# Optimization experiments

Hardware: AMD Instinct MI355X
Metric: run time of the kernel (lower is better)

The kernel has to match this reference:

```python
import jax, jax.numpy as jnp
import numpy as np

L_NOOBJ = 3.0


def _scale_loss(pred, gt, modulus, mask_pos, mask_neg):
    # pred/gt: [B,H,W,A,5+C]; modulus: [B,H,W,A,6]; mask_pos: [B,H,W,A] bool; mask_neg: same shape as pred, bool
    C = pred.shape[-1] - 5
    mpos = mask_pos.astype(pred.dtype)[..., None]           # broadcast over channel dim
    n_pos = jnp.sum(mask_pos)
    n_pos_f = jnp.maximum(n_pos, 1).astype(pred.dtype)
    # modulus weight of the LAST positive cell (reproduces box_param[ground_index][0] after the loop)
    flat = mask_pos.reshape(-1)
    idx_last = flat.shape[0] - 1 - jnp.argmax(flat[::-1])
    w_last = modulus.reshape(-1, 6)[idx_last, 0]
    diff2 = (gt - pred) ** 2 * mpos
    coord = w_last * jnp.sum(diff2[..., 0:4]) / n_pos_f
    conf_pos = jnp.sum(diff2[..., 4]) / n_pos_f
    # BCEWithLogitsLoss (mean over selected rows x C elements), numerically stable form
    x = pred[..., 5:]
    z = gt[..., 5:]
    bce = jnp.maximum(x, 0.0) - x * z + jnp.log1p(jnp.exp(-jnp.abs(x)))
    classify = jnp.sum(bce * mpos) / (n_pos_f * C)
    pos_loss = jnp.where(n_pos > 0, coord + conf_pos + classify, 0.0)
    # negative: elementwise masked MSE over full tensor, scaled by l_noobj
    mneg = mask_neg.astype(pred.dtype)
    n_neg = jnp.sum(mask_neg)
    neg = L_NOOBJ * jnp.sum(((gt - pred) ** 2) * mneg) / jnp.maximum(n_neg, 1).astype(pred.dtype)
    neg_loss = jnp.where(n_neg > 0, neg, 0.0)
    return pos_loss + neg_loss


def setup_inputs() -> dict:
    key = jax.random.key(0)
    B, A, C = 16, 3, 80
    sizes = {"small": 76, "middle": 38, "big": 19}
    out = {}
    k = key
    for name, g in sizes.items():
        k, k1, k2, k3, k4, k5 = jax.random.split(k, 6)
        out[f"{name}_pred"] = jax.random.normal(k1, (B, g, g, A, 5 + C), dtype=jnp.float32)
        out[f"{name}_gt"] = jax.random.uniform(k2, (B, g, g, A, 5 + C), dtype=jnp.float32)
        out[f"{name}_modulus"] = jax.random.uniform(k3, (B, g, g, A, 6), dtype=jnp.float32) + 0.5
        out[f"{name}_mask_pos"] = jax.random.bernoulli(k4, 0.01, (B, g, g, A))
        out[f"{name}_mask_neg"] = jax.random.bernoulli(k5, 0.3, (B, g, g, A, 5 + C))
    return out


def reference(small_pred, small_gt, small_modulus, small_mask_pos, small_mask_neg,
              middle_pred, middle_gt, middle_modulus, middle_mask_pos, middle_mask_neg,
              big_pred, big_gt, big_modulus, big_mask_pos, big_mask_neg):
    loss = (_scale_loss(small_pred, small_gt, small_modulus, small_mask_pos, small_mask_neg)
            + _scale_loss(middle_pred, middle_gt, middle_modulus, middle_mask_pos, middle_mask_neg)
            + _scale_loss(big_pred, big_gt, big_modulus, big_mask_pos, big_mask_neg))
    return loss
```

## Files before the change

kernel.cpp:

```cpp
#include <hip/hip_runtime.h>

typedef unsigned int u32;
typedef unsigned long long u64;

#define NG0 5891520u
#define NG1 1472880u
#define NG2 368220u
#define NC0 277248u
#define NC1 69312u
#define NC2 17328u
#define NBLK 2048u
#define PB0 1083u
#define PB1 271u
#define PB2 68u
#define PBTOT (PB0 + PB1 + PB2)

struct NegAcc { float sn; u32 nn; };
struct PosAcc { float sc, sf, sb; u32 np, mi, pad[3]; };


__device__ __forceinline__ void neg_body(const float4 pv, const float4 gv,
                                         const int4 mv, float& sn, u32& nn)
{
  float d;
  d = gv.x - pv.x; sn = fmaf(d * d, (float)mv.x, sn); nn += (u32)mv.x;
  d = gv.y - pv.y; sn = fmaf(d * d, (float)mv.y, sn); nn += (u32)mv.y;
  d = gv.z - pv.z; sn = fmaf(d * d, (float)mv.z, sn); nn += (u32)mv.z;
  d = gv.w - pv.w; sn = fmaf(d * d, (float)mv.w, sn); nn += (u32)mv.w;
}

__device__ __forceinline__ void neg_scale(
    const float* __restrict__ pred, const float* __restrict__ gt,
    const int* __restrict__ mneg, u32 n, u32 tid, u32 stride,
    NegAcc* __restrict__ slot)
{
  const float4* __restrict__ p4 = (const float4*)pred;
  const float4* __restrict__ g4 = (const float4*)gt;
  const int4*   __restrict__ m4 = (const int4*)mneg;
  float sn = 0.f; u32 nn = 0;
  const u32 iters = n / stride;
  u32 i = 0;
  for (; i + 4 <= iters; i += 4) {
    u32 g0 = tid + i * stride, g1 = g0 + stride, g2 = g1 + stride, g3 = g2 + stride;
    float4 pa = p4[g0], pb = p4[g1], pc = p4[g2], pd = p4[g3];
    float4 qa = g4[g0], qb = g4[g1], qc = g4[g2], qd = g4[g3];
    int4   ma = m4[g0], mb = m4[g1], mc = m4[g2], md = m4[g3];
    neg_body(pa, qa, ma, sn, nn);
    neg_body(pb, qb, mb, sn, nn);
    neg_body(pc, qc, mc, sn, nn);
    neg_body(pd, qd, md, sn, nn);
  }
  for (; i < iters; ++i) {
    u32 ga = tid + i * stride;
    neg_body(p4[ga], g4[ga], m4[ga], sn, nn);
  }
  u32 gl = tid + iters * stride;
  if (gl < n) {
    neg_body(p4[gl], g4[gl], m4[gl], sn, nn);
  }
  #pragma unroll
  for (int o = 32; o > 0; o >>= 1) {
    sn += __shfl_down(sn, o);
    nn += __shfl_down((int)nn, o);
  }
  __shared__ float shf[4];
  __shared__ u32 shu[4];
  const int wave = threadIdx.x >> 6, lane = threadIdx.x & 63;
  if (lane == 0) { shf[wave] = sn; shu[wave] = nn; }
  __syncthreads();
  if (threadIdx.x == 0) {
    NegAcc a;
    a.sn = shf[0] + shf[1] + shf[2] + shf[3];
    a.nn = shu[0] + shu[1] + shu[2] + shu[3];
    *slot = a;
  }
  __syncthreads();
}

__global__ __launch_bounds__(256) void yolo_neg(
    const float* __restrict__ pred0, const float* __restrict__ gt0, const int* __restrict__ mn0,
    const float* __restrict__ pred1, const float* __restrict__ gt1, const int* __restrict__ mn1,
    const float* __restrict__ pred2, const float* __restrict__ gt2, const int* __restrict__ mn2,
    NegAcc* __restrict__ neg)
{
  const u32 tid = blockIdx.x * blockDim.x + threadIdx.x;
  const u32 stride = gridDim.x * blockDim.x;
  neg_scale(pred0, gt0, mn0, NG0, tid, stride, &neg[0 * NBLK + blockIdx.x]);
  neg_scale(pred1, gt1, mn1, NG1, tid, stride, &neg[1 * NBLK + blockIdx.x]);
  neg_scale(pred2, gt2, mn2, NG2, tid, stride, &neg[2 * NBLK + blockIdx.x]);
}


__global__ __launch_bounds__(256) void yolo_pos(
    const float* __restrict__ pred0, const float* __restrict__ gt0, const int* __restrict__ mp0,
    const float* __restrict__ pred1, const float* __restrict__ gt1, const int* __restrict__ mp1,
    const float* __restrict__ pred2, const float* __restrict__ gt2, const int* __restrict__ mp2,
    PosAcc* __restrict__ pos)
{
  const u32 b = blockIdx.x;
  const float* pred; const float* gtp; const int* mp; u32 nc, cell0;
  if (b < PB0)            { pred = pred0; gtp = gt0; mp = mp0; nc = NC0; cell0 = b * 256u; }
  else if (b < PB0 + PB1) { pred = pred1; gtp = gt1; mp = mp1; nc = NC1; cell0 = (b - PB0) * 256u; }
  else                    { pred = pred2; gtp = gt2; mp = mp2; nc = NC2; cell0 = (b - PB0 - PB1) * 256u; }

  const int lane = threadIdx.x & 63;
  const int wave = threadIdx.x >> 6;
  const u32 cell = cell0 + threadIdx.x;
  const u32 wavecell0 = cell0 + (u32)(threadIdx.x & ~63u);

  const bool active = (cell < nc) && (mp[cell] != 0);
  u64 bal = __ballot(active);

  float sc = 0.f, sf = 0.f, sb = 0.f;
  u32 np = active ? 1u : 0u;
  u32 mi = active ? cell : 0u;

  while (bal) {
    const int src = __ffsll(bal) - 1;
    bal &= bal - 1ull;
    const u32 c = wavecell0 + (u32)src;
    const float* __restrict__ pp = pred + (size_t)c * 85u;
    const float* __restrict__ gg = gtp  + (size_t)c * 85u;
    float x0 = pp[lane], z0 = gg[lane];
    float d0 = z0 - x0;
    float b0 = fmaxf(x0, 0.f) - x0 * z0 + __logf(1.f + __expf(-fabsf(x0)));
    if (lane < 4)       sc += d0 * d0;
    else if (lane == 4) sf += d0 * d0;
    else                sb += b0;
    if (lane < 21) {
      float x1 = pp[64 + lane], z1 = gg[64 + lane];
      sb += fmaxf(x1, 0.f) - x1 * z1 + __logf(1.f + __expf(-fabsf(x1)));
    }
  }

  #pragma unroll
  for (int o = 32; o > 0; o >>= 1) {
    sc += __shfl_down(sc, o);
    sf += __shfl_down(sf, o);
    sb += __shfl_down(sb, o);
    np += __shfl_down((int)np, o);
    u32 om = __shfl_down((int)mi, o);
    mi = om > mi ? om : mi;
  }
  __shared__ float shf[3][4];
  __shared__ u32 shu[2][4];
  if (lane == 0) {
    shf[0][wave] = sc; shf[1][wave] = sf; shf[2][wave] = sb;
    shu[0][wave] = np; shu[1][wave] = mi;
  }
  __syncthreads();
  if (threadIdx.x == 0) {
    PosAcc a = {0.f, 0.f, 0.f, 0u, 0u, {0u, 0u, 0u}};
    #pragma unroll
    for (int w = 0; w < 4; ++w) {
      a.sc += shf[0][w]; a.sf += shf[1][w]; a.sb += shf[2][w];
      a.np += shu[0][w];
      a.mi = shu[1][w] > a.mi ? shu[1][w] : a.mi;
    }
    pos[b] = a;
  }
}


__global__ __launch_bounds__(256) void yolo_final(
    const NegAcc* __restrict__ neg, const PosAcc* __restrict__ pos,
    const float* __restrict__ mod0, const float* __restrict__ mod1,
    const float* __restrict__ mod2, float* __restrict__ out)
{
  const float* mods[3] = {mod0, mod1, mod2};
  const u32 pbase[3] = {0u, PB0, PB0 + PB1};
  const u32 pcnt[3]  = {PB0, PB1, PB2};
  __shared__ float shf[4][4];
  __shared__ u32 shu[3][4];
  const int wave = threadIdx.x >> 6, lane = threadIdx.x & 63;
  float loss = 0.f;
  for (int s = 0; s < 3; ++s) {
    float sn = 0.f, sc = 0.f, sf = 0.f, sb = 0.f;
    u32 nn = 0, np = 0, mi = 0;
    for (u32 t = threadIdx.x; t < NBLK; t += 256u) {
      NegAcc a = neg[(u32)s * NBLK + t];
      sn += a.sn; nn += a.nn;
    }
    for (u32 t = threadIdx.x; t < pcnt[s]; t += 256u) {
      PosAcc a = pos[pbase[s] + t];
      sc += a.sc; sf += a.sf; sb += a.sb; np += a.np;
      mi = a.mi > mi ? a.mi : mi;
    }
    #pragma unroll
    for (int o = 32; o > 0; o >>= 1) {
      sn += __shfl_down(sn, o);
      sc += __shfl_down(sc, o);
      sf += __shfl_down(sf, o);
      sb += __shfl_down(sb, o);
      nn += __shfl_down((int)nn, o);
      np += __shfl_down((int)np, o);
      u32 om = __shfl_down((int)mi, o);
      mi = om > mi ? om : mi;
    }
    if (lane == 0) {
      shf[0][wave] = sn; shf[1][wave] = sc; shf[2][wave] = sf; shf[3][wave] = sb;
      shu[0][wave] = nn; shu[1][wave] = np; shu[2][wave] = mi;
    }
    __syncthreads();
    if (threadIdx.x == 0) {
      float Sn = 0.f, Sc = 0.f, Sf = 0.f, Sb = 0.f;
      u32 Nn = 0, Np = 0, Mi = 0;
      #pragma unroll
      for (int w = 0; w < 4; ++w) {
        Sn += shf[0][w]; Sc += shf[1][w]; Sf += shf[2][w]; Sb += shf[3][w];
        Nn += shu[0][w]; Np += shu[1][w];
        Mi = shu[2][w] > Mi ? shu[2][w] : Mi;
      }
      if (Np > 0u) {
        float w_last = mods[s][(size_t)Mi * 6u];
        loss += (w_last * Sc + Sf + Sb * (1.f / 80.f)) / (float)Np;
      }
      if (Nn > 0u) loss += 3.0f * Sn / (float)Nn;
    }
    __syncthreads();
  }
  if (threadIdx.x == 0) out[0] = loss;
}

extern "C" void kernel_launch(void* const* d_in, const int* in_sizes, int n_in,
                              void* d_out, int out_size, void* d_ws, size_t ws_size,
                              hipStream_t stream)
{
  const float* pred0 = (const float*)d_in[0];
  const float* gt0   = (const float*)d_in[1];
  const float* mod0  = (const float*)d_in[2];
  const int*   mp0   = (const int*)d_in[3];
  const int*   mn0   = (const int*)d_in[4];
  const float* pred1 = (const float*)d_in[5];
  const float* gt1   = (const float*)d_in[6];
  const float* mod1  = (const float*)d_in[7];
  const int*   mp1   = (const int*)d_in[8];
  const int*   mn1   = (const int*)d_in[9];
  const float* pred2 = (const float*)d_in[10];
  const float* gt2   = (const float*)d_in[11];
  const float* mod2  = (const float*)d_in[12];
  const int*   mp2   = (const int*)d_in[13];
  const int*   mn2   = (const int*)d_in[14];

  NegAcc* neg = (NegAcc*)d_ws;
  PosAcc* pos = (PosAcc*)((char*)d_ws + 3 * NBLK * sizeof(NegAcc));

  yolo_neg<<<NBLK, 256, 0, stream>>>(pred0, gt0, mn0,
                                     pred1, gt1, mn1,
                                     pred2, gt2, mn2, neg);
  yolo_pos<<<PBTOT, 256, 0, stream>>>(pred0, gt0, mp0,
                                      pred1, gt1, mp1,
                                      pred2, gt2, mp2, pos);
  yolo_final<<<1, 256, 0, stream>>>(neg, pos, mod0, mod1, mod2, (float*)d_out);
}
```

Before: 88.64 us.

## Fuse negative and positive loss kernels into one launch with single-wave finalize

After: 86.43 us. 1.03x faster.

```diff
diff --git a/kernel.cpp b/kernel.cpp
--- a/kernel.cpp
+++ b/kernel.cpp
@@ -15,9 +15,13 @@
 #define PB2 68u
 #define PBTOT (PB0 + PB1 + PB2)
 
-struct NegAcc { float sn; u32 nn; };
-struct PosAcc { float sc, sf, sb; u32 np, mi, pad[3]; };
-
+struct BlockAcc {
+  float sn0, sn1, sn2;
+  u32   nn0, nn1, nn2;
+  float sc, sf, sb;
+  u32   np, mi;
+  u32   pad[5];
+};
 
 __device__ __forceinline__ void neg_body(const float4 pv, const float4 gv,
                                          const int4 mv, float& sn, u32& nn)
@@ -29,197 +33,185 @@
   d = gv.w - pv.w; sn = fmaf(d * d, (float)mv.w, sn); nn += (u32)mv.w;
 }
 
-__device__ __forceinline__ void neg_scale(
+__device__ __forceinline__ void neg_stream(
     const float* __restrict__ pred, const float* __restrict__ gt,
     const int* __restrict__ mneg, u32 n, u32 tid, u32 stride,
-    NegAcc* __restrict__ slot)
+    float& sn, u32& nn)
 {
   const float4* __restrict__ p4 = (const float4*)pred;
   const float4* __restrict__ g4 = (const float4*)gt;
   const int4*   __restrict__ m4 = (const int4*)mneg;
-  float sn = 0.f; u32 nn = 0;
   const u32 iters = n / stride;
   u32 i = 0;
-  for (; i + 4 <= iters; i += 4) {
-    u32 g0 = tid + i * stride, g1 = g0 + stride, g2 = g1 + stride, g3 = g2 + stride;
-    float4 pa = p4[g0], pb = p4[g1], pc = p4[g2], pd = p4[g3];
-    float4 qa = g4[g0], qb = g4[g1], qc = g4[g2], qd = g4[g3];
-    int4   ma = m4[g0], mb = m4[g1], mc = m4[g2], md = m4[g3];
+  for (; i + 2 <= iters; i += 2) {
+    u32 ga = tid + i * stride, gb = ga + stride;
+    float4 pa = p4[ga], qa = g4[ga]; int4 ma = m4[ga];
+    float4 pb = p4[gb], qb = g4[gb]; int4 mb = m4[gb];
     neg_body(pa, qa, ma, sn, nn);
     neg_body(pb, qb, mb, sn, nn);
-    neg_body(pc, qc, mc, sn, nn);
-    neg_body(pd, qd, md, sn, nn);
-  }
-  for (; i < iters; ++i) {
+  }
+  if (i < iters) {
     u32 ga = tid + i * stride;
     neg_body(p4[ga], g4[ga], m4[ga], sn, nn);
   }
   u32 gl = tid + iters * stride;
-  if (gl < n) {
-    neg_body(p4[gl], g4[gl], m4[gl], sn, nn);
-  }
+  if (gl < n) neg_body(p4[gl], g4[gl], m4[gl], sn, nn);
+}
+
+__global__ __launch_bounds__(256) void yolo_fused(
+    const float* __restrict__ pred0, const float* __restrict__ gt0,
+    const int* __restrict__ mp0, const int* __restrict__ mn0,
+    const float* __restrict__ pred1, const float* __restrict__ gt1,
+    const int* __restrict__ mp1, const int* __restrict__ mn1,
+    const float* __restrict__ pred2, const float* __restrict__ gt2,
+    const int* __restrict__ mp2, const int* __restrict__ mn2,
+    BlockAcc* __restrict__ ws)
+{
+  const u32 tid = blockIdx.x * blockDim.x + threadIdx.x;
+  const u32 stride = gridDim.x * blockDim.x;
+
+  float sn0 = 0.f, sn1 = 0.f, sn2 = 0.f;
+  u32 nn0 = 0, nn1 = 0, nn2 = 0;
+  neg_stream(pred0, gt0, mn0, NG0, tid, stride, sn0, nn0);
+  neg_stream(pred1, gt1, mn1, NG1, tid, stride, sn1, nn1);
+  neg_stream(pred2, gt2, mn2, NG2, tid, stride, sn2, nn2);
+
+  float sc = 0.f, sf = 0.f, sb = 0.f;
+  u32 np = 0, mi = 0;
+  const u32 b = blockIdx.x;
+  if (b < PBTOT) {
+    const float* pred; const float* gtp; const int* mp; u32 nc, cell0;
+    if (b < PB0)            { pred = pred0; gtp = gt0; mp = mp0; nc = NC0; cell0 = b * 256u; }
+    else if (b < PB0 + PB1) { pred = pred1; gtp = gt1; mp = mp1; nc = NC1; cell0 = (b - PB0) * 256u; }
+    else                    { pred = pred2; gtp = gt2; mp = mp2; nc = NC2; cell0 = (b - PB0 - PB1) * 256u; }
+
+    const int lane = threadIdx.x & 63;
+    const u32 cell = cell0 + threadIdx.x;
+    const u32 wavecell0 = cell0 + (u32)(threadIdx.x & ~63u);
+    const bool active = (cell < nc) && (mp[cell] != 0);
+    u64 bal = __ballot(active);
+    np = active ? 1u : 0u;
+    mi = active ? cell : 0u;
+
+    while (bal) {
+      const int src = __ffsll(bal) - 1;
+      bal &= bal - 1ull;
+      const u32 c = wavecell0 + (u32)src;
+      const float* __restrict__ pp = pred + (size_t)c * 85u;
+      const float* __restrict__ gg = gtp  + (size_t)c * 85u;
+      float x0 = pp[lane], z0 = gg[lane];
+      float d0 = z0 - x0;
+      float b0 = fmaxf(x0, 0.f) - x0 * z0 + __logf(1.f + __expf(-fabsf(x0)));
+      if (lane < 4)       sc += d0 * d0;
+      else if (lane == 4) sf += d0 * d0;
+      else                sb += b0;
+      if (lane < 21) {
+        float x1 = pp[64 + lane], z1 = gg[64 + lane];
+        sb += fmaxf(x1, 0.f) - x1 * z1 + __logf(1.f + __expf(-fabsf(x1)));
+      }
+    }
+  }
+
   #pragma unroll
   for (int o = 32; o > 0; o >>= 1) {
-    sn += __shfl_down(sn, o);
-    nn += __shfl_down((int)nn, o);
-  }
-  __shared__ float shf[4];
-  __shared__ u32 shu[4];
+    sn0 += __shfl_down(sn0, o);
+    sn1 += __shfl_down(sn1, o);
+    sn2 += __shfl_down(sn2, o);
+    nn0 += __shfl_down((int)nn0, o);
+    nn1 += __shfl_down((int)nn1, o);
+    nn2 += __shfl_down((int)nn2, o);
+    sc  += __shfl_down(sc, o);
+    sf  += __shfl_down(sf, o);
+    sb  += __shfl_down(sb, o);
+    np  += __shfl_down((int)np, o);
+    u32 om = __shfl_down((int)mi, o);
+    mi = om > mi ? om : mi;
+  }
+  __shared__ float shf[6][4];
+  __shared__ u32 shu[5][4];
   const int wave = threadIdx.x >> 6, lane = threadIdx.x & 63;
-  if (lane == 0) { shf[wave] = sn; shu[wave] = nn; }
+  if (lane == 0) {
+    shf[0][wave] = sn0; shf[1][wave] = sn1; shf[2][wave] = sn2;
+    shf[3][wave] = sc;  shf[4][wave] = sf;  shf[5][wave] = sb;
+    shu[0][wave] = nn0; shu[1][wave] = nn1; shu[2][wave] = nn2;
+    shu[3][wave] = np;  shu[4][wave] = mi;
+  }
   __syncthreads();
   if (threadIdx.x == 0) {
-    NegAcc a;
-    a.sn = shf[0] + shf[1] + shf[2] + shf[3];
-    a.nn = shu[0] + shu[1] + shu[2] + shu[3];
-    *slot = a;
-  }
-  __syncthreads();
-}
-
-__global__ __launch_bounds__(256) void yolo_neg(
-    const float* __restrict__ pred0, const float* __restrict__ gt0, const int* __restrict__ mn0,
-    const float* __restrict__ pred1, const float* __restrict__ gt1, const int* __restrict__ mn1,
-    const float* __restrict__ pred2, const float* __restrict__ gt2, const int* __restrict__ mn2,
-    NegAcc* __restrict__ neg)
-{
-  const u32 tid = blockIdx.x * blockDim.x + threadIdx.x;
-  const u32 stride = gridDim.x * blockDim.x;
-  neg_scale(pred0, gt0, mn0, NG0, tid, stride, &neg[0 * NBLK + blockIdx.x]);
-  neg_scale(pred1, gt1, mn1, NG1, tid, stride, &neg[1 * NBLK + blockIdx.x]);
-  neg_scale(pred2, gt2, mn2, NG2, tid, stride, &neg[2 * NBLK + blockIdx.x]);
-}
-
-
-__global__ __launch_bounds__(256) void yolo_pos(
-    const float* __restrict__ pred0, const float* __restrict__ gt0, const int* __restrict__ mp0,
-    const float* __restrict__ pred1, const float* __restrict__ gt1, const int* __restrict__ mp1,
-    const float* __restrict__ pred2, const float* __restrict__ gt2, const int* __restrict__ mp2,
-    PosAcc* __restrict__ pos)
-{
-  const u32 b = blockIdx.x;
-  const float* pred; const float* gtp; const int* mp; u32 nc, cell0;
-  if (b < PB0)            { pred = pred0; gtp = gt0; mp = mp0; nc = NC0; cell0 = b * 256u; }
-  else if (b < PB0 + PB1) { pred = pred1; gtp = gt1; mp = mp1; nc = NC1; cell0 = (b - PB0) * 256u; }
-  else                    { pred = pred2; gtp = gt2; mp = mp2; nc = NC2; cell0 = (b - PB0 - PB1) * 256u; }
-
-  const int lane = threadIdx.x & 63;
-  const int wave = threadIdx.x >> 6;
-  const u32 cell = cell0 + threadIdx.x;
-  const u32 wavecell0 = cell0 + (u32)(threadIdx.x & ~63u);
-
-  const bool active = (cell < nc) && (mp[cell] != 0);
-  u64 bal = __ballot(active);
-
-  float sc = 0.f, sf = 0.f, sb = 0.f;
-  u32 np = active ? 1u : 0u;
-  u32 mi = active ? cell : 0u;
-
-  while (bal) {
-    const int src = __ffsll(bal) - 1;
-    bal &= bal - 1ull;
-    const u32 c = wavecell0 + (u32)src;
-    const float* __restrict__ pp = pred + (size_t)c * 85u;
-    const float* __restrict__ gg = gtp  + (size_t)c * 85u;
-    float x0 = pp[lane], z0 = gg[lane];
-    float d0 = z0 - x0;
-    float b0 = fmaxf(x0, 0.f) - x0 * z0 + __logf(1.f + __expf(-fabsf(x0)));
-    if (lane < 4)       sc += d0 * d0;
-    else if (lane == 4) sf += d0 * d0;
-    else                sb += b0;
-    if (lane < 21) {
-      float x1 = pp[64 + lane], z1 = gg[64 + lane];
-      sb += fmaxf(x1, 0.f) - x1 * z1 + __logf(1.f + __expf(-fabsf(x1)));
+    BlockAcc a = {};
+    #pragma unroll
+    for (int w = 0; w < 4; ++w) {
+      a.sn0 += shf[0][w]; a.sn1 += shf[1][w]; a.sn2 += shf[2][w];
+      a.sc  += shf[3][w]; a.sf  += shf[4][w]; a.sb  += shf[5][w];
+      a.nn0 += shu[0][w]; a.nn1 += shu[1][w]; a.nn2 += shu[2][w];
+      a.np  += shu[3][w];
+      a.mi = shu[4][w] > a.mi ? shu[4][w] : a.mi;
     }
+    ws[blockIdx.x] = a;
+  }
+}
+
+__global__ __launch_bounds__(64) void yolo_final(
+    const BlockAcc* __restrict__ ws,
+    const float* __restrict__ mod0, const float* __restrict__ mod1,
+    const float* __restrict__ mod2, float* __restrict__ out)
+{
+  const int lane = threadIdx.x;
+  float sn0 = 0.f, sn1 = 0.f, sn2 = 0.f;
+  float nn0 = 0.f, nn1 = 0.f, nn2 = 0.f;
+  u32 in0 = 0, in1 = 0, in2 = 0;
+  for (u32 t = lane; t < NBLK; t += 64u) {
+    const BlockAcc a = ws[t];
+    sn0 += a.sn0; sn1 += a.sn1; sn2 += a.sn2;
+    in0 += a.nn0; in1 += a.nn1; in2 += a.nn2;
+  }
+  nn0 = (float)in0; nn1 = (float)in1; nn2 = (float)in2;
+
+  float sc0 = 0.f, sf0 = 0.f, sb0 = 0.f; u32 np0 = 0, mi0 = 0;
+  for (u32 t = lane; t < PB0; t += 64u) {
+    const BlockAcc a = ws[t];
+    sc0 += a.sc; sf0 += a.sf; sb0 += a.sb; np0 += a.np;
+    mi0 = a.mi > mi0 ? a.mi : mi0;
+  }
+  float sc1 = 0.f, sf1 = 0.f, sb1 = 0.f; u32 np1 = 0, mi1 = 0;
+  for (u32 t = PB0 + lane; t < PB0 + PB1; t += 64u) {
+    const BlockAcc a = ws[t];
+    sc1 += a.sc; sf1 += a.sf; sb1 += a.sb; np1 += a.np;
+    mi1 = a.mi > mi1 ? a.mi : mi1;
+  }
+  float sc2 = 0.f, sf2 = 0.f, sb2 = 0.f; u32 np2 = 0, mi2 = 0;
+  for (u32 t = PB0 + PB1 + lane; t < PBTOT; t += 64u) {
+    const BlockAcc a = ws[t];
+    sc2 += a.sc; sf2 += a.sf; sb2 += a.sb; np2 += a.np;
+    mi2 = a.mi > mi2 ? a.mi : mi2;
   }
 
   #pragma unroll
   for (int o = 32; o > 0; o >>= 1) {
-    sc += __shfl_down(sc, o);
-    sf += __shfl_down(sf, o);
-    sb += __shfl_down(sb, o);
-    np += __shfl_down((int)np, o);
-    u32 om = __shfl_down((int)mi, o);
-    mi = om > mi ? om : mi;
-  }
-  __shared__ float shf[3][4];
-  __shared__ u32 shu[2][4];
+    sn0 += __shfl_down(sn0, o); sn1 += __shfl_down(sn1, o); sn2 += __shfl_down(sn2, o);
+    nn0 += __shfl_down(nn0, o); nn1 += __shfl_down(nn1, o); nn2 += __shfl_down(nn2, o);
+    sc0 += __shfl_down(sc0, o); sf0 += __shfl_down(sf0, o); sb0 += __shfl_down(sb0, o);
+    sc1 += __shfl_down(sc1, o); sf1 += __shfl_down(sf1, o); sb1 += __shfl_down(sb1, o);
+    sc2 += __shfl_down(sc2, o); sf2 += __shfl_down(sf2, o); sb2 += __shfl_down(sb2, o);
+    np0 += __shfl_down((int)np0, o); np1 += __shfl_down((int)np1, o); np2 += __shfl_down((int)np2, o);
+    u32 m0 = __shfl_down((int)mi0, o); mi0 = m0 > mi0 ? m0 : mi0;
+    u32 m1 = __shfl_down((int)mi1, o); mi1 = m1 > mi1 ? m1 : mi1;
+    u32 m2 = __shfl_down((int)mi2, o); mi2 = m2 > mi2 ? m2 : mi2;
+  }
+
   if (lane == 0) {
-    shf[0][wave] = sc; shf[1][wave] = sf; shf[2][wave] = sb;
-    shu[0][wave] = np; shu[1][wave] = mi;
-  }
-  __syncthreads();
-  if (threadIdx.x == 0) {
-    PosAcc a = {0.f, 0.f, 0.f, 0u, 0u, {0u, 0u, 0u}};
-    #pragma unroll
-    for (int w = 0; w < 4; ++w) {
-      a.sc += shf[0][w]; a.sf += shf[1][w]; a.sb += shf[2][w];
-      a.np += shu[0][w];
-      a.mi = shu[1][w] > a.mi ? shu[1][w] : a.mi;
-    }
-    pos[b] = a;
-  }
-}
-
-
-__global__ __launch_bounds__(256) void yolo_final(
-    const NegAcc* __restrict__ neg, const PosAcc* __restrict__ pos,
-    const float* __restrict__ mod0, const float* __restrict__ mod1,
-    const float* __restrict__ mod2, float* __restrict__ out)
-{
-  const float* mods[3] = {mod0, mod1, mod2};
-  const u32 pbase[3] = {0u, PB0, PB0 + PB1};
-  const u32 pcnt[3]  = {PB0, PB1, PB2};
-  __shared__ float shf[4][4];
-  __shared__ u32 shu[3][4];
-  const int wave = threadIdx.x >> 6, lane = threadIdx.x & 63;
-  float loss = 0.f;
-  for (int s = 0; s < 3; ++s) {
-    float sn = 0.f, sc = 0.f, sf = 0.f, sb = 0.f;
-    u32 nn = 0, np = 0, mi = 0;
-    for (u32 t = threadIdx.x; t < NBLK; t += 256u) {
-      NegAcc a = neg[(u32)s * NBLK + t];
-      sn += a.sn; nn += a.nn;
-    }
-    for (u32 t = threadIdx.x; t < pcnt[s]; t += 256u) {
-      PosAcc a = pos[pbase[s] + t];
-      sc += a.sc; sf += a.sf; sb += a.sb; np += a.np;
-      mi = a.mi > mi ? a.mi : mi;
-    }
-    #pragma unroll
-    for (int o = 32; o > 0; o >>= 1) {
-      sn += __shfl_down(sn, o);
-      sc += __shfl_down(sc, o);
-      sf += __shfl_down(sf, o);
-      sb += __shfl_down(sb, o);
-      nn += __shfl_down((int)nn, o);
-      np += __shfl_down((int)np, o);
-      u32 om = __shfl_down((int)mi, o);
-      mi = om > mi ? om : mi;
-    }
-    if (lane == 0) {
-      shf[0][wave] = sn; shf[1][wave] = sc; shf[2][wave] = sf; shf[3][wave] = sb;
-      shu[0][wave] = nn; shu[1][wave] = np; shu[2][wave] = mi;
-    }
-    __syncthreads();
-    if (threadIdx.x == 0) {
-      float Sn = 0.f, Sc = 0.f, Sf = 0.f, Sb = 0.f;
-      u32 Nn = 0, Np = 0, Mi = 0;
-      #pragma unroll
-      for (int w = 0; w < 4; ++w) {
-        Sn += shf[0][w]; Sc += shf[1][w]; Sf += shf[2][w]; Sb += shf[3][w];
-        Nn += shu[0][w]; Np += shu[1][w];
-        Mi = shu[2][w] > Mi ? shu[2][w] : Mi;
-      }
-      if (Np > 0u) {
-        float w_last = mods[s][(size_t)Mi * 6u];
-        loss += (w_last * Sc + Sf + Sb * (1.f / 80.f)) / (float)Np;
-      }
-      if (Nn > 0u) loss += 3.0f * Sn / (float)Nn;
-    }
-    __syncthreads();
-  }
-  if (threadIdx.x == 0) out[0] = loss;
+    float loss = 0.f;
+    if (np0 > 0u)
+      loss += (mod0[(size_t)mi0 * 6u] * sc0 + sf0 + sb0 * (1.f / 80.f)) / (float)np0;
+    if (nn0 > 0.f) loss += 3.0f * sn0 / nn0;
+    if (np1 > 0u)
+      loss += (mod1[(size_t)mi1 * 6u] * sc1 + sf1 + sb1 * (1.f / 80.f)) / (float)np1;
+    if (nn1 > 0.f) loss += 3.0f * sn1 / nn1;
+    if (np2 > 0u)
+      loss += (mod2[(size_t)mi2 * 6u] * sc2 + sf2 + sb2 * (1.f / 80.f)) / (float)np2;
+    if (nn2 > 0.f) loss += 3.0f * sn2 / nn2;
+    out[0] = loss;
+  }
 }
 
 extern "C" void kernel_launch(void* const* d_in, const int* in_sizes, int n_in,
@@ -242,14 +234,10 @@
   const int*   mp2   = (const int*)d_in[13];
   const int*   mn2   = (const int*)d_in[14];
 
-  NegAcc* neg = (NegAcc*)d_ws;
-  PosAcc* pos = (PosAcc*)((char*)d_ws + 3 * NBLK * sizeof(NegAcc));
-
-  yolo_neg<<<NBLK, 256, 0, stream>>>(pred0, gt0, mn0,
-                                     pred1, gt1, mn1,
-                                     pred2, gt2, mn2, neg);
-  yolo_pos<<<PBTOT, 256, 0, stream>>>(pred0, gt0, mp0,
-                                      pred1, gt1, mp1,
-                                      pred2, gt2, mp2, pos);
-  yolo_final<<<1, 256, 0, stream>>>(neg, pos, mod0, mod1, mod2, (float*)d_out);
-}
+  BlockAcc* ws = (BlockAcc*)d_ws;
+
+  yolo_fused<<<NBLK, 256, 0, stream>>>(pred0, gt0, mp0, mn0,
+                                       pred1, gt1, mp1, mn1,
+                                       pred2, gt2, mp2, mn2, ws);
+  yolo_final<<<1, 64, 0, stream>>>(ws, mod0, mod1, mod2, (float*)d_out);
+}
```
